# Performance work log

Measured on AMD Instinct MI355X. Metric: run time of the kernel, lower is better.

## Reference

```python
import jax, jax.numpy as jnp
import numpy as np

_W1 = np.array([[[-1, 0, 0], [0, 1, 0], [0, 0, 0]],
                [[0, -1, 0], [0, 1, 0], [0, 0, 0]],
                [[0, 0, -1], [0, 1, 0], [0, 0, 0]],
                [[0, 0, 0], [-1, 1, 0], [0, 0, 0]]], dtype=np.float32).reshape(4, 1, 3, 3)
_W2 = _W1[:, :, ::-1, ::-1].copy()

BN_EPS = 1e-3  # YOLOX BaseConv BatchNorm eps
SHIFTS = (1, 3)


def _conv1x1(x, w, b=None):
    # x: (B,C,H,W), w: (O,C,1,1)
    y = jnp.einsum('bchw,oc->bohw', x, w[:, :, 0, 0])
    if b is not None:
        y = y + b[None, :, None, None]
    return y


def _grouped_dilated(x, w, d, groups):
    # 3x3 grouped conv, dilation d, 'same' padding (pad = d for 3x3)
    return jax.lax.conv_general_dilated(
        x, w, window_strides=(1, 1), padding=((d, d), (d, d)),
        rhs_dilation=(d, d), dimension_numbers=('NCHW', 'OIHW', 'NCHW'),
        feature_group_count=groups)


def setup_inputs() -> dict:
    key = jax.random.key(0)
    ks = jax.random.split(key, 6)
    B, C, H, W = 4, 128, 384, 384
    Cq = C // 4
    return {
        'cen': jax.random.normal(ks[0], (B, C, H, W), jnp.float32),
        'mas': jax.random.normal(ks[1], (B, 1, H, W), jnp.float32),
        'scales': jnp.zeros((4,), jnp.float32),
        'in_conv_w': jax.random.normal(ks[2], (Cq, C, 1, 1), jnp.float32) * 0.05,
        'in_conv_b': jnp.zeros((Cq,), jnp.float32),
        'base_w': jax.random.normal(ks[3], (Cq, Cq, 1, 1), jnp.float32) * 0.1,
        'bn_gamma': jnp.ones((Cq,), jnp.float32),
        'bn_beta': jnp.zeros((Cq,), jnp.float32),
        'bn_mean': jnp.zeros((Cq,), jnp.float32),
        'bn_var': jnp.ones((Cq,), jnp.float32),
        'out_w': jax.random.normal(ks[4], (1, Cq, 1, 1), jnp.float32) * 0.1,
        'out_b': jnp.zeros((1,), jnp.float32),
    }


def reference(cen, mas, scales, in_conv_w, in_conv_b, base_w,
              bn_gamma, bn_beta, bn_mean, bn_var, out_w, out_b):
    B, C, H, W = cen.shape
    Cq = C // 4
    k1 = jnp.asarray(np.tile(_W1, (Cq, 1, 1, 1)))  # (4*Cq,1,3,3)
    k2 = jnp.asarray(np.tile(_W2, (Cq, 1, 1, 1)))

    x = _conv1x1(cen, in_conv_w, in_conv_b)  # (B,Cq,H,W)
    outs = []
    for shift in SHIFTS:
        o1 = _grouped_dilated(x, k1, shift, Cq)  # (B,4*Cq,H,W)
        o2 = _grouped_dilated(x, k2, shift, Cq)
        o = (o1 * o2).reshape(B, Cq, 4, H, W).min(axis=2)
        outs.append(o)
    outs = jnp.stack(outs, axis=-1)  # (B,Cq,H,W,n_shifts)
    feat = jax.nn.relu(outs.max(axis=-1) + outs.mean(axis=-1))

    # out_conv = BaseConv(1x1, BN, SiLU) + Conv2d(Cq->1, 1x1)
    y = _conv1x1(feat, base_w)
    inv = jax.lax.rsqrt(bn_var + BN_EPS)
    y = (y - bn_mean[None, :, None, None]) * (bn_gamma * inv)[None, :, None, None] + bn_beta[None, :, None, None]
    y = jax.nn.silu(y)
    att = jax.nn.sigmoid(_conv1x1(y, out_w, out_b))  # (B,1,H,W)

    s = jax.nn.softmax(scales)
    m = jax.nn.sigmoid(mas)
    return cen * (att * m * s[0] + m * s[1] + s[2] * att + s[3])
```

## Files before the change

kernel.cpp:

```cpp
#include <hip/hip_runtime.h>

#define HH 384
#define WW 384
#define HWSZ (HH*WW)
#define CIN 128
#define CQ 32
#define NB 4
#define NPIX (NB*HWSZ)

__device__ __forceinline__ float sigmoidf_(float v){ return 1.0f/(1.0f + __expf(-v)); }

__global__ __launch_bounds__(256) void k_conv1(const float* __restrict__ cen,
    const float* __restrict__ wmat, const float* __restrict__ bvec,
    float* __restrict__ x) {
  __shared__ float wl[CIN*CQ];
  int t = threadIdx.x;
  for (int i = t; i < CIN*CQ; i += 256) {
    int c = i >> 5, o = i & 31;
    wl[i] = wmat[o*CIN + c];
  }
  __syncthreads();
  int p0  = blockIdx.x * 512 + t*2;
  int b   = p0 / HWSZ;
  int pix = p0 - b*HWSZ;
  const float* cb = cen + (size_t)b*CIN*HWSZ + pix;
  float2 acc[CQ];
  #pragma unroll
  for (int o=0;o<CQ;o++){ acc[o].x=0.f; acc[o].y=0.f; }
  #pragma unroll 2
  for (int c=0;c<CIN;c+=4){
    float2 v0 = *(const float2*)(cb + (size_t)(c+0)*HWSZ);
    float2 v1 = *(const float2*)(cb + (size_t)(c+1)*HWSZ);
    float2 v2 = *(const float2*)(cb + (size_t)(c+2)*HWSZ);
    float2 v3 = *(const float2*)(cb + (size_t)(c+3)*HWSZ);
    #pragma unroll
    for (int o=0;o<CQ;o++){
      float w0 = wl[(c+0)*CQ+o], w1 = wl[(c+1)*CQ+o];
      float w2 = wl[(c+2)*CQ+o], w3 = wl[(c+3)*CQ+o];
      acc[o].x = fmaf(v0.x,w0,acc[o].x); acc[o].y = fmaf(v0.y,w0,acc[o].y);
      acc[o].x = fmaf(v1.x,w1,acc[o].x); acc[o].y = fmaf(v1.y,w1,acc[o].y);
      acc[o].x = fmaf(v2.x,w2,acc[o].x); acc[o].y = fmaf(v2.y,w2,acc[o].y);
      acc[o].x = fmaf(v3.x,w3,acc[o].x); acc[o].y = fmaf(v3.y,w3,acc[o].y);
    }
  }
  float* xb = x + (size_t)b*CQ*HWSZ + pix;
  #pragma unroll
  for (int o=0;o<CQ;o++){
    float bb = bvec[o];
    float2 r; r.x = acc[o].x + bb; r.y = acc[o].y + bb;
    *(float2*)(xb + (size_t)o*HWSZ) = r;
  }
}

#define TH 4
#define TW 64
#define LDSW 72
#define LDSN 720
#define GBX 6
#define GBY 96

__global__ __launch_bounds__(256) void k_att(const float* __restrict__ x,
    const float* __restrict__ mas, const float* __restrict__ scales,
    const float* __restrict__ base_w,
    const float* __restrict__ bn_g, const float* __restrict__ bn_b,
    const float* __restrict__ bn_m, const float* __restrict__ bn_v,
    const float* __restrict__ out_w, const float* __restrict__ out_b,
    float* __restrict__ a_out) {
  __shared__ float bwl[CQ*CQ];
  __shared__ float ows[CQ], bns[CQ], bnsh[CQ];
  __shared__ float tile[2][LDSN];
  int t = threadIdx.x;
  for (int i=t;i<CQ*CQ;i+=256) bwl[i] = base_w[i];
  if (t < CQ) {
    float inv = rsqrtf(bn_v[t] + 1e-3f);
    float g = bn_g[t]*inv;
    bns[t]  = g;
    bnsh[t] = bn_b[t] - bn_m[t]*g;
    ows[t]  = out_w[t];
  }

  int gid = blockIdx.x;
  int b   = gid / (GBX*GBY);
  int rem = gid - b*(GBX*GBY);
  int ty  = rem / GBX;
  int tx  = rem - ty*GBX;
  int h0  = ty*TH, w0 = tx*TW;

  int soff[3]; float sval[3];
  #pragma unroll
  for (int j=0;j<3;j++){
    int i = t + j*256;
    int r = i / LDSW, cc = i - r*LDSW;
    int hh = h0 - 3 + r, wq = w0 - 3 + cc;
    bool ok = (i < LDSN) && (cc < 70) &&
              ((unsigned)hh < (unsigned)HH) && ((unsigned)wq < (unsigned)WW);
    soff[j] = ok ? (hh*WW + wq) : 0;
    sval[j] = ok ? 1.0f : 0.0f;
  }

  int rr  = t >> 6, cc2 = t & 63;
  const int cbase = (3+rr)*LDSW + 3 + cc2;
  const float* xb = x + (size_t)b*CQ*HWSZ;

  float y[CQ];
  #pragma unroll
  for (int o=0;o<CQ;o++) y[o] = 0.f;

  __syncthreads();

  #pragma unroll 2
  for (int c=0;c<CQ;c++){
    float* buf = tile[c&1];
    const float* xc = xb + (size_t)c*HWSZ;
    #pragma unroll
    for (int j=0;j<3;j++){
      int i = t + j*256;
      if (i < LDSN) buf[i] = sval[j] * xc[soff[j]];
    }
    __syncthreads();
    const float* p = buf + cbase;
    float xv = p[0];
    float q0 = (xv-p[-LDSW-1])*(xv-p[ LDSW+1]);
    float q1 = (xv-p[-LDSW  ])*(xv-p[ LDSW  ]);
    float q2 = (xv-p[-LDSW+1])*(xv-p[ LDSW-1]);
    float q3 = (xv-p[-1     ])*(xv-p[ 1     ]);
    float os0 = fminf(fminf(q0,q1),fminf(q2,q3));
    float r0 = (xv-p[-3*LDSW-3])*(xv-p[ 3*LDSW+3]);
    float r1 = (xv-p[-3*LDSW  ])*(xv-p[ 3*LDSW  ]);
    float r2 = (xv-p[-3*LDSW+3])*(xv-p[ 3*LDSW-3]);
    float r3 = (xv-p[-3      ])*(xv-p[ 3       ]);
    float os1 = fminf(fminf(r0,r1),fminf(r2,r3));
    float v = fmaxf(os0,os1) + 0.5f*(os0+os1);
    float fc = fmaxf(v, 0.0f);
    #pragma unroll
    for (int o=0;o<CQ;o++) y[o] = fmaf(fc, bwl[o*CQ+c], y[o]);
  }

  float att_lin = out_b[0];
  #pragma unroll
  for (int o=0;o<CQ;o++){
    float yy = y[o]*bns[o] + bnsh[o];
    att_lin += ows[o]*(yy*sigmoidf_(yy));
  }
  float att = sigmoidf_(att_lin);

  float s0=scales[0],s1=scales[1],s2=scales[2],s3=scales[3];
  float mx = fmaxf(fmaxf(s0,s1),fmaxf(s2,s3));
  float e0=__expf(s0-mx), e1=__expf(s1-mx), e2=__expf(s2-mx), e3=__expf(s3-mx);
  float inv = 1.0f/(e0+e1+e2+e3);
  int p_out = b*HWSZ + (h0+rr)*WW + (w0+cc2);
  float m = sigmoidf_(mas[p_out]);
  a_out[p_out] = (att*m)*(e0*inv) + m*(e1*inv) + att*(e2*inv) + (e3*inv);
}

__global__ __launch_bounds__(256) void k_out(const float* __restrict__ cen,
    const float* __restrict__ a, float* __restrict__ out){
  unsigned i = blockIdx.x*256u + threadIdx.x;
  unsigned e = i*4u;
  unsigned bc  = e / HWSZ;
  unsigned pix = e - bc*HWSZ;
  unsigned b   = bc >> 7;
  float4 v  = ((const float4*)cen)[i];
  float4 av = ((const float4*)a)[(b*HWSZ + pix) >> 2];
  float4 r;
  r.x = v.x*av.x; r.y = v.y*av.y; r.z = v.z*av.z; r.w = v.w*av.w;
  ((float4*)out)[i] = r;
}

extern "C" void kernel_launch(void* const* d_in, const int* in_sizes, int n_in,
                              void* d_out, int out_size, void* d_ws, size_t ws_size,
                              hipStream_t stream) {
  const float* cen    = (const float*)d_in[0];
  const float* mas    = (const float*)d_in[1];
  const float* scales = (const float*)d_in[2];
  const float* in_w   = (const float*)d_in[3];
  const float* in_b   = (const float*)d_in[4];
  const float* base_w = (const float*)d_in[5];
  const float* bn_g   = (const float*)d_in[6];
  const float* bn_b   = (const float*)d_in[7];
  const float* bn_m   = (const float*)d_in[8];
  const float* bn_v   = (const float*)d_in[9];
  const float* out_w  = (const float*)d_in[10];
  const float* out_b  = (const float*)d_in[11];
  float* out = (float*)d_out;

  float* x = (float*)d_ws;
  float* a = x + (size_t)NB*CQ*HWSZ;

  k_conv1<<<NPIX/512, 256, 0, stream>>>(cen, in_w, in_b, x);
  k_att  <<<NB*GBX*GBY, 256, 0, stream>>>(x, mas, scales, base_w,
                                          bn_g, bn_b, bn_m, bn_v, out_w, out_b, a);
  k_out  <<<(NB*CIN*HWSZ)/1024, 256, 0, stream>>>(cen, a, out);
}
```

Measured before the change: 728.9 us.

## Precompute weights in prep kernel, read uniform weights from global, double att tile height

A single-block prep kernel now transposes the conv weights and folds the BN, out-conv and softmax parameters into a workspace buffer once per call. The conv1 and att kernels then read these weights through uniform global loads, likely scalar loads, instead of staging them in shared memory with a barrier. The att kernel's tile height goes from 4 to 8 rows, so each thread computes two output pixels and the 3-pixel halo loads are shared across more rows. In exchange it adds a kernel launch, more registers per thread in att and conv1, and makes weight access depend on the compiler turning it into scalar loads.

Measured after the change: 698.4 us. 1.04x faster.

```diff
diff --git a/kernel.cpp b/kernel.cpp
--- a/kernel.cpp
+++ b/kernel.cpp
@@ -10,16 +10,37 @@
 
 __device__ __forceinline__ float sigmoidf_(float v){ return 1.0f/(1.0f + __expf(-v)); }
 
+__global__ __launch_bounds__(256) void k_prep(
+    const float* __restrict__ in_w, const float* __restrict__ base_w,
+    const float* __restrict__ bn_g, const float* __restrict__ bn_b,
+    const float* __restrict__ bn_m, const float* __restrict__ bn_v,
+    const float* __restrict__ out_w, const float* __restrict__ out_b,
+    const float* __restrict__ scales,
+    float* __restrict__ wt, float* __restrict__ bt, float* __restrict__ prm){
+  int t = threadIdx.x;
+  for (int i = t; i < CIN*CQ; i += 256){ int c = i >> 5, o = i & 31; wt[i] = in_w[o*CIN + c]; }
+  for (int i = t; i < CQ*CQ;  i += 256){ int c = i >> 5, o = i & 31; bt[i] = base_w[o*CQ + c]; }
+  if (t < CQ){
+    float inv = rsqrtf(bn_v[t] + 1e-3f);
+    float g = bn_g[t]*inv;
+    prm[t]      = g;
+    prm[32 + t] = bn_b[t] - bn_m[t]*g;
+    prm[64 + t] = out_w[t];
+  }
+  if (t == 0){
+    float s0=scales[0], s1=scales[1], s2=scales[2], s3=scales[3];
+    float mx = fmaxf(fmaxf(s0,s1), fmaxf(s2,s3));
+    float e0=expf(s0-mx), e1=expf(s1-mx), e2=expf(s2-mx), e3=expf(s3-mx);
+    float inv = 1.0f/(e0+e1+e2+e3);
+    prm[96]=e0*inv; prm[97]=e1*inv; prm[98]=e2*inv; prm[99]=e3*inv;
+    prm[100]=out_b[0];
+  }
+}
+
 __global__ __launch_bounds__(256) void k_conv1(const float* __restrict__ cen,
-    const float* __restrict__ wmat, const float* __restrict__ bvec,
+    const float* __restrict__ wt, const float* __restrict__ bvec,
     float* __restrict__ x) {
-  __shared__ float wl[CIN*CQ];
   int t = threadIdx.x;
-  for (int i = t; i < CIN*CQ; i += 256) {
-    int c = i >> 5, o = i & 31;
-    wl[i] = wmat[o*CIN + c];
-  }
-  __syncthreads();
   int p0  = blockIdx.x * 512 + t*2;
   int b   = p0 / HWSZ;
   int pix = p0 - b*HWSZ;
@@ -28,19 +49,14 @@
   #pragma unroll
   for (int o=0;o<CQ;o++){ acc[o].x=0.f; acc[o].y=0.f; }
   #pragma unroll 2
-  for (int c=0;c<CIN;c+=4){
-    float2 v0 = *(const float2*)(cb + (size_t)(c+0)*HWSZ);
-    float2 v1 = *(const float2*)(cb + (size_t)(c+1)*HWSZ);
-    float2 v2 = *(const float2*)(cb + (size_t)(c+2)*HWSZ);
-    float2 v3 = *(const float2*)(cb + (size_t)(c+3)*HWSZ);
+  for (int c=0;c<CIN;c++){
+    float2 v = *(const float2*)(cb + (size_t)c*HWSZ);
+    const float* wc = wt + c*CQ;
     #pragma unroll
     for (int o=0;o<CQ;o++){
-      float w0 = wl[(c+0)*CQ+o], w1 = wl[(c+1)*CQ+o];
-      float w2 = wl[(c+2)*CQ+o], w3 = wl[(c+3)*CQ+o];
-      acc[o].x = fmaf(v0.x,w0,acc[o].x); acc[o].y = fmaf(v0.y,w0,acc[o].y);
-      acc[o].x = fmaf(v1.x,w1,acc[o].x); acc[o].y = fmaf(v1.y,w1,acc[o].y);
-      acc[o].x = fmaf(v2.x,w2,acc[o].x); acc[o].y = fmaf(v2.y,w2,acc[o].y);
-      acc[o].x = fmaf(v3.x,w3,acc[o].x); acc[o].y = fmaf(v3.y,w3,acc[o].y);
+      float w = wc[o];
+      acc[o].x = fmaf(v.x, w, acc[o].x);
+      acc[o].y = fmaf(v.y, w, acc[o].y);
     }
   }
   float* xb = x + (size_t)b*CQ*HWSZ + pix;
@@ -52,32 +68,34 @@
   }
 }
 
-#define TH 4
+#define TH 8
 #define TW 64
 #define LDSW 72
-#define LDSN 720
+#define LDSN (14*LDSW)
 #define GBX 6
-#define GBY 96
+#define GBY 48
+
+__device__ __forceinline__ float stencil_eval(const float* p){
+  float xv = p[0];
+  float q0 = (xv-p[-LDSW-1])*(xv-p[ LDSW+1]);
+  float q1 = (xv-p[-LDSW  ])*(xv-p[ LDSW  ]);
+  float q2 = (xv-p[-LDSW+1])*(xv-p[ LDSW-1]);
+  float q3 = (xv-p[-1     ])*(xv-p[ 1     ]);
+  float os0 = fminf(fminf(q0,q1),fminf(q2,q3));
+  float r0 = (xv-p[-3*LDSW-3])*(xv-p[ 3*LDSW+3]);
+  float r1 = (xv-p[-3*LDSW  ])*(xv-p[ 3*LDSW  ]);
+  float r2 = (xv-p[-3*LDSW+3])*(xv-p[ 3*LDSW-3]);
+  float r3 = (xv-p[-3      ])*(xv-p[ 3       ]);
+  float os1 = fminf(fminf(r0,r1),fminf(r2,r3));
+  float v = fmaxf(os0,os1) + 0.5f*(os0+os1);
+  return fmaxf(v, 0.0f);
+}
 
 __global__ __launch_bounds__(256) void k_att(const float* __restrict__ x,
-    const float* __restrict__ mas, const float* __restrict__ scales,
-    const float* __restrict__ base_w,
-    const float* __restrict__ bn_g, const float* __restrict__ bn_b,
-    const float* __restrict__ bn_m, const float* __restrict__ bn_v,
-    const float* __restrict__ out_w, const float* __restrict__ out_b,
-    float* __restrict__ a_out) {
-  __shared__ float bwl[CQ*CQ];
-  __shared__ float ows[CQ], bns[CQ], bnsh[CQ];
+    const float* __restrict__ mas, const float* __restrict__ bt,
+    const float* __restrict__ prm, float* __restrict__ a_out) {
   __shared__ float tile[2][LDSN];
   int t = threadIdx.x;
-  for (int i=t;i<CQ*CQ;i+=256) bwl[i] = base_w[i];
-  if (t < CQ) {
-    float inv = rsqrtf(bn_v[t] + 1e-3f);
-    float g = bn_g[t]*inv;
-    bns[t]  = g;
-    bnsh[t] = bn_b[t] - bn_m[t]*g;
-    ows[t]  = out_w[t];
-  }
 
   int gid = blockIdx.x;
   int b   = gid / (GBX*GBY);
@@ -86,9 +104,9 @@
   int tx  = rem - ty*GBX;
   int h0  = ty*TH, w0 = tx*TW;
 
-  int soff[3]; float sval[3];
-  #pragma unroll
-  for (int j=0;j<3;j++){
+  int soff[4]; float sval[4];
+  #pragma unroll
+  for (int j=0;j<4;j++){
     int i = t + j*256;
     int r = i / LDSW, cc = i - r*LDSW;
     int hh = h0 - 3 + r, wq = w0 - 3 + cc;
@@ -99,58 +117,54 @@
   }
 
   int rr  = t >> 6, cc2 = t & 63;
-  const int cbase = (3+rr)*LDSW + 3 + cc2;
+  const int cbase0 = (3+rr)*LDSW + 3 + cc2;
+  const int cbase1 = cbase0 + 4*LDSW;
   const float* xb = x + (size_t)b*CQ*HWSZ;
 
-  float y[CQ];
-  #pragma unroll
-  for (int o=0;o<CQ;o++) y[o] = 0.f;
-
-  __syncthreads();
+  float y0[CQ], y1[CQ];
+  #pragma unroll
+  for (int o=0;o<CQ;o++){ y0[o]=0.f; y1[o]=0.f; }
 
   #pragma unroll 2
   for (int c=0;c<CQ;c++){
     float* buf = tile[c&1];
     const float* xc = xb + (size_t)c*HWSZ;
     #pragma unroll
-    for (int j=0;j<3;j++){
+    for (int j=0;j<4;j++){
       int i = t + j*256;
       if (i < LDSN) buf[i] = sval[j] * xc[soff[j]];
     }
     __syncthreads();
-    const float* p = buf + cbase;
-    float xv = p[0];
-    float q0 = (xv-p[-LDSW-1])*(xv-p[ LDSW+1]);
-    float q1 = (xv-p[-LDSW  ])*(xv-p[ LDSW  ]);
-    float q2 = (xv-p[-LDSW+1])*(xv-p[ LDSW-1]);
-    float q3 = (xv-p[-1     ])*(xv-p[ 1     ]);
-    float os0 = fminf(fminf(q0,q1),fminf(q2,q3));
-    float r0 = (xv-p[-3*LDSW-3])*(xv-p[ 3*LDSW+3]);
-    float r1 = (xv-p[-3*LDSW  ])*(xv-p[ 3*LDSW  ]);
-    float r2 = (xv-p[-3*LDSW+3])*(xv-p[ 3*LDSW-3]);
-    float r3 = (xv-p[-3      ])*(xv-p[ 3       ]);
-    float os1 = fminf(fminf(r0,r1),fminf(r2,r3));
-    float v = fmaxf(os0,os1) + 0.5f*(os0+os1);
-    float fc = fmaxf(v, 0.0f);
+    float fc0 = stencil_eval(buf + cbase0);
+    float fc1 = stencil_eval(buf + cbase1);
+    const float* wc = bt + c*CQ;
     #pragma unroll
-    for (int o=0;o<CQ;o++) y[o] = fmaf(fc, bwl[o*CQ+c], y[o]);
-  }
-
-  float att_lin = out_b[0];
+    for (int o=0;o<CQ;o++){
+      float w = wc[o];
+      y0[o] = fmaf(fc0, w, y0[o]);
+      y1[o] = fmaf(fc1, w, y1[o]);
+    }
+  }
+
+  float w0p=prm[96], w1p=prm[97], w2p=prm[98], w3p=prm[99], ob=prm[100];
+  float lin0=ob, lin1=ob;
   #pragma unroll
   for (int o=0;o<CQ;o++){
-    float yy = y[o]*bns[o] + bnsh[o];
-    att_lin += ows[o]*(yy*sigmoidf_(yy));
-  }
-  float att = sigmoidf_(att_lin);
-
-  float s0=scales[0],s1=scales[1],s2=scales[2],s3=scales[3];
-  float mx = fmaxf(fmaxf(s0,s1),fmaxf(s2,s3));
-  float e0=__expf(s0-mx), e1=__expf(s1-mx), e2=__expf(s2-mx), e3=__expf(s3-mx);
-  float inv = 1.0f/(e0+e1+e2+e3);
-  int p_out = b*HWSZ + (h0+rr)*WW + (w0+cc2);
-  float m = sigmoidf_(mas[p_out]);
-  a_out[p_out] = (att*m)*(e0*inv) + m*(e1*inv) + att*(e2*inv) + (e3*inv);
+    float g=prm[o], sh=prm[32+o], ow=prm[64+o];
+    float yy0 = fmaf(y0[o], g, sh);
+    float yy1 = fmaf(y1[o], g, sh);
+    lin0 = fmaf(ow*yy0, sigmoidf_(yy0), lin0);
+    lin1 = fmaf(ow*yy1, sigmoidf_(yy1), lin1);
+  }
+  float att0 = sigmoidf_(lin0);
+  float att1 = sigmoidf_(lin1);
+
+  int pa = b*HWSZ + (h0+rr)*WW + (w0+cc2);
+  int pc = pa + 4*WW;
+  float m0 = sigmoidf_(mas[pa]);
+  float m1 = sigmoidf_(mas[pc]);
+  a_out[pa] = (att0*m0)*w0p + m0*w1p + att0*w2p + w3p;
+  a_out[pc] = (att1*m1)*w0p + m1*w1p + att1*w2p + w3p;
 }
 
 __global__ __launch_bounds__(256) void k_out(const float* __restrict__ cen,
@@ -184,11 +198,15 @@
   const float* out_b  = (const float*)d_in[11];
   float* out = (float*)d_out;
 
-  float* x = (float*)d_ws;
-  float* a = x + (size_t)NB*CQ*HWSZ;
-
-  k_conv1<<<NPIX/512, 256, 0, stream>>>(cen, in_w, in_b, x);
-  k_att  <<<NB*GBX*GBY, 256, 0, stream>>>(x, mas, scales, base_w,
-                                          bn_g, bn_b, bn_m, bn_v, out_w, out_b, a);
+  float* x   = (float*)d_ws;
+  float* a   = x  + (size_t)NB*CQ*HWSZ;
+  float* wt  = a  + (size_t)NB*HWSZ;
+  float* bt  = wt + (size_t)CIN*CQ;
+  float* prm = bt + (size_t)CQ*CQ;
+
+  k_prep <<<1, 256, 0, stream>>>(in_w, base_w, bn_g, bn_b, bn_m, bn_v,
+                                 out_w, out_b, scales, wt, bt, prm);
+  k_conv1<<<NPIX/512, 256, 0, stream>>>(cen, wt, in_b, x);
+  k_att  <<<NB*GBX*GBY, 256, 0, stream>>>(x, mas, bt, prm, a);
   k_out  <<<(NB*CIN*HWSZ)/1024, 256, 0, stream>>>(cen, a, out);
 }
```
